# Kernel tuning notes

Measured on AMD Instinct MI355X. Metric: run time of the kernel, lower is better.

## Reference

```python
import jax, jax.numpy as jnp
import numpy as np

EMBED_DIM = 1024
NUM_HEADS = 16
LB_HEADS = 8
LA_HEADS = 8
HEAD_DIM = EMBED_DIM // NUM_HEADS


def setup_inputs() -> dict:
    key = jax.random.key(0)
    ks = jax.random.split(key, 8)
    B, T, F, D = 2, 16, 128, EMBED_DIM
    def xavier(k, shape):
        fan_out, fan_in = shape[-2], shape[-1]
        lim = float(np.sqrt(6.0 / (fan_in + fan_out)))
        return jax.random.uniform(k, shape, jnp.float32, -lim, lim)
    return {
        "x": jax.random.normal(ks[0], (B, T, F, D), jnp.float32),
        # stacked per-head Linear weights, torch layout (out=head_dim, in=D)
        "Wq_lb": xavier(ks[1], (LB_HEADS, HEAD_DIM, D)),
        "Wk_lb": xavier(ks[2], (LB_HEADS, HEAD_DIM, D)),
        "Wv_lb": xavier(ks[3], (LB_HEADS, HEAD_DIM, D)),
        "Wq_la": xavier(ks[4], (LA_HEADS, HEAD_DIM, D)),
        "Wk_la": xavier(ks[5], (LA_HEADS, HEAD_DIM, D)),
        "Wv_la": xavier(ks[6], (LA_HEADS, HEAD_DIM, D)),
        "Wo": xavier(ks[7], (D, D)),
    }


def _masked_attention(xf, Wq, Wk, Wv, lookahead):
    # xf: (B, N, D); W*: (H, E, D). Equivalent to per-head Linear then stack.
    q = jnp.einsum('bnd,hed->bhne', xf, Wq)
    k = jnp.einsum('bnd,hed->bhne', xf, Wk)
    v = jnp.einsum('bnd,hed->bhne', xf, Wv)
    scale = 1.0 / jnp.sqrt(jnp.asarray(q.shape[-1], q.dtype))
    s = jnp.einsum('bhqe,bhke->bhqk', q, k) * scale
    n = s.shape[-1]
    i = jnp.arange(n)
    # frame/patch divmod mask reduces to token-level (anti-)causal
    mask = (i[:, None] <= i[None, :]) if lookahead else (i[:, None] >= i[None, :])
    s = jnp.where(mask, s, jnp.finfo(s.dtype).min)
    p = jax.nn.softmax(s, axis=-1)
    return jnp.einsum('bhqk,bhke->bhqe', p, v)  # (B, H, N, E)


def reference(x, Wq_lb, Wk_lb, Wv_lb, Wq_la, Wk_la, Wv_la, Wo):
    B, T, F, D = x.shape
    xf = x.reshape(B, T * F, D)
    o_lb = _masked_attention(xf, Wq_lb, Wk_lb, Wv_lb, lookahead=False)
    o_la = _masked_attention(xf, Wq_la, Wk_la, Wv_la, lookahead=True)
    o = jnp.concatenate([o_lb, o_la], axis=1)          # (B, H, N, E)
    o = o.reshape(B, T * F, D)                          # NOTE: raw reshape, no head transpose (matches torch source)
    out = jnp.einsum('bnd,od->bno', o, Wo)
    return out.reshape(B, T, F, D)
```

## Files before the change

### kernel.cpp

```cpp
#include <hip/hip_runtime.h>
#include <hip/hip_bf16.h>

constexpr int B_    = 2;
constexpr int NTOK  = 2048;
constexpr int D_    = 1024;
constexpr int H_    = 16;
constexpr int E_    = 64;

using bf16_t = __bf16;
using bf16x8 = __attribute__((ext_vector_type(8))) __bf16;
using bf16x4 = __attribute__((ext_vector_type(4))) __bf16;
using f32x4  = __attribute__((ext_vector_type(4))) float;

#define NEG_BIG  (-30000.0f)
#define QSCALE   (0.125f * 1.44269504088896f)

__device__ __forceinline__ void load16_to_lds(const void* g, void* l) {
  __builtin_amdgcn_global_load_lds((const __attribute__((address_space(1))) void*)g,
                                   (__attribute__((address_space(3))) void*)l, 16, 0, 0);
}

__device__ __forceinline__ void stage64_async(const bf16_t* __restrict__ g, int gs,
                                              bf16_t* l, int tid) {
#pragma unroll
  for (int j = 0; j < 2; ++j) {
    int chunk = j * 256 + tid;
    int row = chunk >> 3, cc = chunk & 7;
    int gcc = cc ^ (row & 7);
    load16_to_lds(g + (long)row * gs + gcc * 8, l + chunk * 8);
  }
}

__device__ __forceinline__ void stage128x64_async(const bf16_t* __restrict__ g, int gs,
                                                  bf16_t* l, int tid) {
#pragma unroll
  for (int j = 0; j < 4; ++j) {
    int chunk = j * 256 + tid;
    int row = chunk >> 3, cc = chunk & 7;
    int gcc = cc ^ (row & 7);
    load16_to_lds(g + (long)row * gs + gcc * 8, l + chunk * 8);
  }
}

__device__ __forceinline__ bf16x8 frag_ld(const bf16_t* l, int row, int ks, int half) {
  int cc = (ks * 4 + half) ^ (row & 7);
  return *(const bf16x8*)&l[row * 64 + cc * 8];
}

__device__ __forceinline__ bf16x8 cvt8(f32x4 f0, f32x4 f1) {
  bf16x8 v;
  v[0] = (bf16_t)f0[0]; v[1] = (bf16_t)f0[1]; v[2] = (bf16_t)f0[2]; v[3] = (bf16_t)f0[3];
  v[4] = (bf16_t)f1[0]; v[5] = (bf16_t)f1[1]; v[6] = (bf16_t)f1[2]; v[7] = (bf16_t)f1[3];
  return v;
}

__device__ __forceinline__ bf16x4 cvt4(f32x4 f, float sc) {
  bf16x4 v;
  v[0] = (bf16_t)(f[0] * sc); v[1] = (bf16_t)(f[1] * sc);
  v[2] = (bf16_t)(f[2] * sc); v[3] = (bf16_t)(f[3] * sc);
  return v;
}

__global__ __launch_bounds__(256) void prep_kernel(
    const float* __restrict__ x,
    const float* __restrict__ q0, const float* __restrict__ q1,
    const float* __restrict__ k0, const float* __restrict__ k1,
    const float* __restrict__ v0, const float* __restrict__ v1,
    const float* __restrict__ wo,
    bf16_t* __restrict__ xb, bf16_t* __restrict__ Wb, bf16_t* __restrict__ Wob)
{
  const int bid = blockIdx.x;
  if (bid < 2048) {
    long i = ((long)bid * 256 + threadIdx.x) * 8;
    *(bf16x8*)&xb[i] = cvt8(*(const f32x4*)&x[i], *(const f32x4*)&x[i + 4]);
  } else if (bid < 3584) {
    int rb = bid - 2048;
    int sec = rb >> 5;
    int qkv = sec >> 4, hh = sec & 15;
    const float* s = (qkv == 0) ? (hh < 8 ? q0 : q1)
                   : (qkv == 1) ? (hh < 8 ? k0 : k1)
                                : (hh < 8 ? v0 : v1);
    s += (long)(hh & 7) * (E_ * D_);
    long off = ((long)(rb & 31) * 256 + threadIdx.x) * 8;
    *(bf16x8*)&Wb[(long)sec * (E_ * D_) + off] =
        cvt8(*(const f32x4*)&s[off], *(const f32x4*)&s[off + 4]);
  } else {
    long i = ((long)(bid - 3584) * 256 + threadIdx.x) * 8;
    *(bf16x8*)&Wob[i] = cvt8(*(const f32x4*)&wo[i], *(const f32x4*)&wo[i + 4]);
  }
}

__global__ __launch_bounds__(256) void qkv128_kernel(
    const bf16_t* __restrict__ xb, const bf16_t* __restrict__ Wb,
    bf16_t* __restrict__ Qb, bf16_t* __restrict__ Kb, bf16_t* __restrict__ Vt)
{
  __shared__ __align__(16) bf16_t smem[2 * 128 * 64];
  bf16_t* As = smem;
  bf16_t* Bs = smem + 128 * 64;

  const int tid = threadIdx.x;
  const int wv = tid >> 6, lane = tid & 63, lane16 = lane & 15, half = lane >> 4;
  const int wm = wv >> 1, wn = wv & 1;
  const int mt = blockIdx.x, nt = blockIdx.y;
  const int sec = nt >> 3;

  const bf16_t* Ag = xb + (long)mt * 128 * D_;
  const bf16_t* Bg = Wb + (long)nt * 128 * D_;

  f32x4 acc[4][4] = {};

  if (sec < 2) {
    for (int k0 = 0; k0 < D_; k0 += 64) {
      __syncthreads();
      stage128x64_async(Ag + k0, D_, As, tid);
      stage128x64_async(Bg + k0, D_, Bs, tid);
      __syncthreads();
#pragma unroll
      for (int ks = 0; ks < 2; ++ks) {
        bf16x8 a[4], b[4];
#pragma unroll
        for (int i = 0; i < 4; ++i) a[i] = frag_ld(As, wm * 64 + i * 16 + lane16, ks, half);
#pragma unroll
        for (int i = 0; i < 4; ++i) b[i] = frag_ld(Bs, wn * 64 + i * 16 + lane16, ks, half);
#pragma unroll
        for (int mi = 0; mi < 4; ++mi)
#pragma unroll
          for (int ni = 0; ni < 4; ++ni)
            acc[mi][ni] = __builtin_amdgcn_mfma_f32_16x16x32_bf16(b[ni], a[mi], acc[mi][ni], 0, 0, 0);
      }
    }
  } else {
    for (int k0 = 0; k0 < D_; k0 += 64) {
      __syncthreads();
      stage128x64_async(Ag + k0, D_, As, tid);
      stage128x64_async(Bg + k0, D_, Bs, tid);
      __syncthreads();
#pragma unroll
      for (int ks = 0; ks < 2; ++ks) {
        bf16x8 a[4], b[4];
#pragma unroll
        for (int i = 0; i < 4; ++i) a[i] = frag_ld(As, wm * 64 + i * 16 + lane16, ks, half);
#pragma unroll
        for (int i = 0; i < 4; ++i) b[i] = frag_ld(Bs, wn * 64 + i * 16 + lane16, ks, half);
#pragma unroll
        for (int mi = 0; mi < 4; ++mi)
#pragma unroll
          for (int ni = 0; ni < 4; ++ni)
            acc[mi][ni] = __builtin_amdgcn_mfma_f32_16x16x32_bf16(a[mi], b[ni], acc[mi][ni], 0, 0, 0);
      }
    }
  }

  const int tok0 = mt * 128;
  const int b  = tok0 >> 11;
  const int n0 = tok0 & 2047;

  if (sec < 2) {
    const float qs = (sec == 0) ? QSCALE : 1.0f;
    bf16_t* dst = (sec == 0) ? Qb : Kb;
#pragma unroll
    for (int mi = 0; mi < 4; ++mi)
#pragma unroll
      for (int ni = 0; ni < 4; ++ni) {
        int token = wm * 64 + 16 * mi + lane16;
        int colg  = nt * 128 + wn * 64 + 16 * ni + half * 4;
        int cs = colg & 1023, hh = cs >> 6, e0 = cs & 63;
        *(bf16x4*)&dst[((long)(b * H_ + hh) * NTOK + n0 + token) * E_ + e0] =
            cvt4(acc[mi][ni], qs);
      }
  } else {
#pragma unroll
    for (int c = 0; c < 2; ++c) {
      __syncthreads();
      if (wn == c) {
#pragma unroll
        for (int mi = 0; mi < 4; ++mi)
#pragma unroll
          for (int ni = 0; ni < 4; ++ni) {
            int t0v = wm * 64 + 16 * mi + half * 4;
            int e   = 16 * ni + lane16;
            *(bf16x4*)&smem[e * 144 + t0v] = cvt4(acc[mi][ni], 1.0f);
          }
      }
      __syncthreads();
      int hh = (nt & 7) * 2 + c;
      bf16_t* vdst = Vt + ((long)(b * H_ + hh) * E_) * NTOK;
#pragma unroll
      for (int q = 0; q < 4; ++q) {
        int chunk = q * 256 + tid;
        int e = chunk >> 4, toff = (chunk & 15) * 8;
        *(bf16x8*)&vdst[(long)e * NTOK + n0 + toff] = *(const bf16x8*)&smem[e * 144 + toff];
      }
    }
  }
}

__global__ __launch_bounds__(256) void attn_kernel(
    const bf16_t* __restrict__ Qb, const bf16_t* __restrict__ Kb,
    const bf16_t* __restrict__ Vt, bf16_t* __restrict__ Ob)
{
  __shared__ __align__(16) bf16_t Kl[2][64 * 64];
  __shared__ __align__(16) bf16_t Vl[2][64 * 64];
  __shared__ __align__(16) bf16_t Pl[2][64 * 72];

  const int tid = threadIdx.x;
  const int wv = tid >> 6, lane = tid & 63, lane16 = lane & 15, half = lane >> 4;
  const int qp = blockIdx.x, h = blockIdx.y, b = blockIdx.z;
  const bool causal = (h < 8);
  const int qb[2] = { qp, 31 - qp };
  const long bh = (long)(b * H_ + h);
  const int qrow = 16 * wv + lane16;

  bf16x8 qf[2][2];
#pragma unroll
  for (int t = 0; t < 2; ++t) {
    const bf16_t* qg = Qb + (bh * NTOK + (long)qb[t] * 64 + qrow) * E_;
    qf[t][0] = *(const bf16x8*)(qg + half * 8);
    qf[t][1] = *(const bf16x8*)(qg + 32 + half * 8);
  }

  f32x4 oacc[2][4] = {};
  float l_acc[2] = { 0.f, 0.f };

  const int lo = causal ? 0 : qp;
  const int hi = causal ? 31 - qp : 31;

  stage64_async(Kb + (bh * NTOK + (long)lo * 64) * E_, E_, Kl[0], tid);
  stage64_async(Vt + bh * E_ * NTOK + (long)lo * 64, NTOK, Vl[0], tid);

  for (int kb = lo; kb <= hi; ++kb) {
    const int cur = (kb - lo) & 1;
    __syncthreads();
    if (kb < hi) {
      stage64_async(Kb + (bh * NTOK + (long)(kb + 1) * 64) * E_, E_, Kl[cur ^ 1], tid);
      stage64_async(Vt + bh * E_ * NTOK + (long)(kb + 1) * 64, NTOK, Vl[cur ^ 1], tid);
    }
    const bool act[2] = { causal ? (kb <= qb[0]) : (kb >= qb[0]),
                          causal ? (kb <= qb[1]) : (kb >= qb[1]) };

    bf16x8 kfr[2][4];
#pragma unroll
    for (int ks = 0; ks < 2; ++ks)
#pragma unroll
      for (int n = 0; n < 4; ++n)
        kfr[ks][n] = frag_ld(Kl[cur], 16 * n + lane16, ks, half);

#pragma unroll
    for (int t = 0; t < 2; ++t) {
      if (!act[t]) continue;
      f32x4 s[4] = {};
#pragma unroll
      for (int ks = 0; ks < 2; ++ks)
#pragma unroll
        for (int n = 0; n < 4; ++n)
          s[n] = __builtin_amdgcn_mfma_f32_16x16x32_bf16(kfr[ks][n], qf[t][ks], s[n], 0, 0, 0);

      if (kb == qb[t]) {
#pragma unroll
        for (int n = 0; n < 4; ++n)
#pragma unroll
          for (int r = 0; r < 4; ++r) {
            int key = 16 * n + half * 4 + r;
            bool ok = causal ? (qrow >= key) : (qrow <= key);
            s[n][r] = ok ? s[n][r] : NEG_BIG;
          }
      }

      float lsum = 0.f;
#pragma unroll
      for (int n = 0; n < 4; ++n)
#pragma unroll
        for (int r = 0; r < 4; ++r) {
          float p = exp2f(s[n][r]);
          s[n][r] = p;
          lsum += p;
        }
      l_acc[t] += lsum;

#pragma unroll
      for (int n = 0; n < 4; ++n)
        *(bf16x4*)&Pl[t][qrow * 72 + 16 * n + half * 4] = cvt4(s[n], 1.0f);
    }
    asm volatile("" ::: "memory");

    bf16x8 vfr[2][4];
#pragma unroll
    for (int ks = 0; ks < 2; ++ks)
#pragma unroll
      for (int n = 0; n < 4; ++n)
        vfr[ks][n] = frag_ld(Vl[cur], 16 * n + lane16, ks, half);

#pragma unroll
    for (int t = 0; t < 2; ++t) {
      if (!act[t]) continue;
      bf16x8 ap0 = *(const bf16x8*)&Pl[t][qrow * 72 + half * 8];
      bf16x8 ap1 = *(const bf16x8*)&Pl[t][qrow * 72 + 32 + half * 8];
#pragma unroll
      for (int n = 0; n < 4; ++n)
        oacc[t][n] = __builtin_amdgcn_mfma_f32_16x16x32_bf16(vfr[0][n], ap0, oacc[t][n], 0, 0, 0);
#pragma unroll
      for (int n = 0; n < 4; ++n)
        oacc[t][n] = __builtin_amdgcn_mfma_f32_16x16x32_bf16(vfr[1][n], ap1, oacc[t][n], 0, 0, 0);
    }
  }

#pragma unroll
  for (int t = 0; t < 2; ++t) {
    l_acc[t] += __shfl_xor(l_acc[t], 16, 64);
    l_acc[t] += __shfl_xor(l_acc[t], 32, 64);
  }

#pragma unroll
  for (int t = 0; t < 2; ++t) {
    float rcp = 1.0f / l_acc[t];
    bf16_t* og = Ob + (bh * NTOK + (long)qb[t] * 64 + qrow) * E_;
#pragma unroll
    for (int n = 0; n < 4; ++n)
      *(bf16x4*)&og[16 * n + half * 4] = cvt4(oacc[t][n], rcp);
  }
}

__global__ __launch_bounds__(256) void oproj128_kernel(
    const bf16_t* __restrict__ Ob, const bf16_t* __restrict__ Wob,
    float* __restrict__ res)
{
  __shared__ __align__(16) bf16_t smem[2 * 128 * 64];
  bf16_t* As = smem;
  bf16_t* Bs = smem + 128 * 64;

  const int tid = threadIdx.x;
  const int wv = tid >> 6, lane = tid & 63, lane16 = lane & 15, half = lane >> 4;
  const int wm = wv >> 1, wn = wv & 1;
  const int mt = blockIdx.x, nt = blockIdx.y;

  const bf16_t* Ag = Ob  + (long)mt * 128 * D_;
  const bf16_t* Bg = Wob + (long)nt * 128 * D_;

  f32x4 acc[4][4] = {};

  for (int k0 = 0; k0 < D_; k0 += 64) {
    __syncthreads();
    stage128x64_async(Ag + k0, D_, As, tid);
    stage128x64_async(Bg + k0, D_, Bs, tid);
    __syncthreads();
#pragma unroll
    for (int ks = 0; ks < 2; ++ks) {
      bf16x8 a[4], b[4];
#pragma unroll
      for (int i = 0; i < 4; ++i) a[i] = frag_ld(As, wm * 64 + i * 16 + lane16, ks, half);
#pragma unroll
      for (int i = 0; i < 4; ++i) b[i] = frag_ld(Bs, wn * 64 + i * 16 + lane16, ks, half);
#pragma unroll
      for (int mi = 0; mi < 4; ++mi)
#pragma unroll
        for (int ni = 0; ni < 4; ++ni)
          acc[mi][ni] = __builtin_amdgcn_mfma_f32_16x16x32_bf16(b[ni], a[mi], acc[mi][ni], 0, 0, 0);
    }
  }

#pragma unroll
  for (int mi = 0; mi < 4; ++mi)
#pragma unroll
    for (int ni = 0; ni < 4; ++ni) {
      int row  = mt * 128 + wm * 64 + 16 * mi + lane16;
      int col0 = nt * 128 + wn * 64 + 16 * ni + half * 4;
      *(f32x4*)&res[(long)row * D_ + col0] = acc[mi][ni];
    }
}

__global__ __launch_bounds__(256) void copy_kernel(const float* __restrict__ src,
                                                   float* __restrict__ dst) {
  long i = ((long)blockIdx.x * 256 + threadIdx.x) * 8;
  *(f32x4*)&dst[i]     = *(const f32x4*)&src[i];
  *(f32x4*)&dst[i + 4] = *(const f32x4*)&src[i + 4];
}

extern "C" void kernel_launch(void* const* d_in, const int* in_sizes, int n_in,
                              void* d_out, int out_size, void* d_ws, size_t ws_size,
                              hipStream_t stream) {
  const float* x     = (const float*)d_in[0];
  const float* wq_lb = (const float*)d_in[1];
  const float* wk_lb = (const float*)d_in[2];
  const float* wv_lb = (const float*)d_in[3];
  const float* wq_la = (const float*)d_in[4];
  const float* wk_la = (const float*)d_in[5];
  const float* wv_la = (const float*)d_in[6];
  const float* wo    = (const float*)d_in[7];
  float* out = (float*)d_out;

  const size_t per_buf = (size_t)B_ * H_ * NTOK * E_;

  bf16_t* Qb = (bf16_t*)d_ws;
  bf16_t* Kb = Qb + per_buf;
  bf16_t* Vt = Kb + per_buf;
  float*  res = (float*)d_ws;

  bf16_t* xb  = (bf16_t*)d_out;
  bf16_t* Wb  = xb + per_buf;
  bf16_t* Wob = Wb + (size_t)3 * 1024 * 1024;
  bf16_t* Ob  = (bf16_t*)d_out;

  prep_kernel<<<4096, 256, 0, stream>>>(x, wq_lb, wq_la, wk_lb, wk_la,
                                        wv_lb, wv_la, wo, xb, Wb, Wob);
  qkv128_kernel<<<dim3(32, 24), 256, 0, stream>>>(xb, Wb, Qb, Kb, Vt);
  attn_kernel<<<dim3(16, 16, 2), 256, 0, stream>>>(Qb, Kb, Vt, Ob);
  oproj128_kernel<<<dim3(32, 8), 256, 0, stream>>>(Ob, Wob, res);
  copy_kernel<<<2048, 256, 0, stream>>>(res, out);
}
```

Baseline: 212.5 us.

## Stage QKV and output-projection stores through LDS and drop the final copy kernel

Q/K epilogues and the output projection epilogue now write accumulator tiles into swizzled shared memory and then issue fully coalesced 16-byte row stores to global memory. When the workspace is large enough, the attention output and bf16 Wo live in workspace so the projection writes directly into the output buffer, removing the separate fp32 copy kernel. The price is extra LDS round-trips and barriers in the epilogues, and a path that depends on workspace size.

```diff
diff --git a/kernel.cpp b/kernel.cpp
--- a/kernel.cpp
+++ b/kernel.cpp
@@ -157,17 +157,29 @@
 
   if (sec < 2) {
     const float qs = (sec == 0) ? QSCALE : 1.0f;
+    bf16_t* L = smem + wn * 8192;
+    __syncthreads();
+#pragma unroll
+    for (int mi = 0; mi < 4; ++mi)
+#pragma unroll
+      for (int ni = 0; ni < 4; ++ni) {
+        int tok = wm * 64 + 16 * mi + lane16;
+        int cc  = (2 * ni + (half >> 1)) ^ (tok & 7);
+        int sub = half & 1;
+        *(bf16x4*)&L[tok * 64 + cc * 8 + sub * 4] = cvt4(acc[mi][ni], qs);
+      }
+    __syncthreads();
     bf16_t* dst = (sec == 0) ? Qb : Kb;
 #pragma unroll
-    for (int mi = 0; mi < 4; ++mi)
-#pragma unroll
-      for (int ni = 0; ni < 4; ++ni) {
-        int token = wm * 64 + 16 * mi + lane16;
-        int colg  = nt * 128 + wn * 64 + 16 * ni + half * 4;
-        int cs = colg & 1023, hh = cs >> 6, e0 = cs & 63;
-        *(bf16x4*)&dst[((long)(b * H_ + hh) * NTOK + n0 + token) * E_ + e0] =
-            cvt4(acc[mi][ni], qs);
-      }
+    for (int j = 0; j < 8; ++j) {
+      int id = j * 256 + tid;
+      int c = id >> 10, rem = id & 1023;
+      int tok = rem >> 3, ec = rem & 7;
+      int scc = ec ^ (tok & 7);
+      bf16x8 v = *(const bf16x8*)&smem[c * 8192 + tok * 64 + scc * 8];
+      int hh = (nt & 7) * 2 + c;
+      *(bf16x8*)&dst[((long)(b * H_ + hh) * NTOK + n0 + tok) * E_ + ec * 8] = v;
+    }
   } else {
 #pragma unroll
     for (int c = 0; c < 2; ++c) {
@@ -358,14 +370,30 @@
     }
   }
 
-#pragma unroll
-  for (int mi = 0; mi < 4; ++mi)
-#pragma unroll
-    for (int ni = 0; ni < 4; ++ni) {
-      int row  = mt * 128 + wm * 64 + 16 * mi + lane16;
-      int col0 = nt * 128 + wn * 64 + 16 * ni + half * 4;
-      *(f32x4*)&res[(long)row * D_ + col0] = acc[mi][ni];
-    }
+  float* Lf = (float*)smem;
+#pragma unroll
+  for (int pass = 0; pass < 2; ++pass) {
+    __syncthreads();
+    if (wn == pass) {
+#pragma unroll
+      for (int mi = 0; mi < 4; ++mi)
+#pragma unroll
+        for (int ni = 0; ni < 4; ++ni) {
+          int tok = wm * 64 + 16 * mi + lane16;
+          int cc  = (4 * ni + half) ^ (tok & 15);
+          *(f32x4*)&Lf[tok * 64 + cc * 4] = acc[mi][ni];
+        }
+    }
+    __syncthreads();
+#pragma unroll
+    for (int j = 0; j < 8; ++j) {
+      int id = j * 256 + tid;
+      int tok = id >> 4, c = id & 15;
+      int cc = c ^ (tok & 15);
+      f32x4 v = *(const f32x4*)&Lf[tok * 64 + cc * 4];
+      *(f32x4*)&res[(long)(mt * 128 + tok) * D_ + nt * 128 + pass * 64 + c * 4] = v;
+    }
+  }
 }
 
 __global__ __launch_bounds__(256) void copy_kernel(const float* __restrict__ src,
@@ -393,17 +421,29 @@
   bf16_t* Qb = (bf16_t*)d_ws;
   bf16_t* Kb = Qb + per_buf;
   bf16_t* Vt = Kb + per_buf;
-  float*  res = (float*)d_ws;
-
-  bf16_t* xb  = (bf16_t*)d_out;
-  bf16_t* Wb  = xb + per_buf;
-  bf16_t* Wob = Wb + (size_t)3 * 1024 * 1024;
-  bf16_t* Ob  = (bf16_t*)d_out;
-
-  prep_kernel<<<4096, 256, 0, stream>>>(x, wq_lb, wq_la, wk_lb, wk_la,
-                                        wv_lb, wv_la, wo, xb, Wb, Wob);
-  qkv128_kernel<<<dim3(32, 24), 256, 0, stream>>>(xb, Wb, Qb, Kb, Vt);
-  attn_kernel<<<dim3(16, 16, 2), 256, 0, stream>>>(Qb, Kb, Vt, Ob);
-  oproj128_kernel<<<dim3(32, 8), 256, 0, stream>>>(Ob, Wob, res);
-  copy_kernel<<<2048, 256, 0, stream>>>(res, out);
-}
+
+  bf16_t* xb = (bf16_t*)d_out;
+  bf16_t* Wb = xb + per_buf;
+
+  const bool direct = ws_size >= (size_t)34 * 1024 * 1024;
+
+  if (direct) {
+    bf16_t* Ob  = Vt + per_buf;
+    bf16_t* Wob = Ob + per_buf;
+    prep_kernel<<<4096, 256, 0, stream>>>(x, wq_lb, wq_la, wk_lb, wk_la,
+                                          wv_lb, wv_la, wo, xb, Wb, Wob);
+    qkv128_kernel<<<dim3(32, 24), 256, 0, stream>>>(xb, Wb, Qb, Kb, Vt);
+    attn_kernel<<<dim3(16, 16, 2), 256, 0, stream>>>(Qb, Kb, Vt, Ob);
+    oproj128_kernel<<<dim3(32, 8), 256, 0, stream>>>(Ob, Wob, out);
+  } else {
+    bf16_t* Wob = Wb + (size_t)3 * 1024 * 1024;
+    bf16_t* Ob  = (bf16_t*)d_out;
+    float*  res = (float*)d_ws;
+    prep_kernel<<<4096, 256, 0, stream>>>(x, wq_lb, wq_la, wk_lb, wk_la,
+                                          wv_lb, wv_la, wo, xb, Wb, Wob);
+    qkv128_kernel<<<dim3(32, 24), 256, 0, stream>>>(xb, Wb, Qb, Kb, Vt);
+    attn_kernel<<<dim3(16, 16, 2), 256, 0, stream>>>(Qb, Kb, Vt, Ob);
+    oproj128_kernel<<<dim3(32, 8), 256, 0, stream>>>(Ob, Wob, res);
+    copy_kernel<<<2048, 256, 0, stream>>>(res, out);
+  }
+}
```

After: 201.4 us. -5.2%, faster.
